# Optimization experiments

Hardware: AMD Instinct MI355X
Metric: run time of the kernel (lower is better)

Reference implementation:

```python
import jax, jax.numpy as jnp
import numpy as np

B, S = 32, 4096
QRYDIM, CTXDIM, ENCDIM = 512, 512, 256


def setup_inputs() -> dict:
    key = jax.random.key(0)
    ks = jax.random.split(key, 8)
    qry = jax.random.normal(ks[0], (B, QRYDIM), dtype=jnp.float32)
    ctx = jax.random.normal(ks[1], (B, S, CTXDIM), dtype=jnp.float32)
    ctx_mask = jax.random.randint(ks[2], (B, S), 0, 2, dtype=jnp.int32)
    # first Linear(qrydim+ctxdim, encdim): split into ctx-part and qry-part
    # (equivalent to concat([ctx, qry]) @ W1^T since concat order is [ctx, qry])
    sc1 = 1.0 / np.sqrt(QRYDIM + CTXDIM)
    Wc = jax.random.uniform(ks[3], (CTXDIM, ENCDIM), jnp.float32, -sc1, sc1)
    Wq = jax.random.uniform(ks[4], (QRYDIM, ENCDIM), jnp.float32, -sc1, sc1)
    b1 = jax.random.uniform(ks[5], (ENCDIM,), jnp.float32, -sc1, sc1)
    sc2 = 1.0 / np.sqrt(ENCDIM)
    w2 = jax.random.uniform(ks[6], (ENCDIM,), jnp.float32, -sc2, sc2)
    b2 = jax.random.uniform(ks[7], (), jnp.float32, -sc2, sc2)
    return {"qry": qry, "ctx": ctx, "ctx_mask": ctx_mask,
            "Wc": Wc, "Wq": Wq, "b1": b1, "w2": w2, "b2": b2}


def reference(qry, ctx, ctx_mask, Wc, Wq, b1, w2, b2):
    # hidden = tanh(concat([ctx, qry_broadcast]) @ W1 + b1), computed without
    # materializing the (B, S, CTXDIM+QRYDIM) concat tensor
    h_ctx = jnp.einsum('bsc,ce->bse', ctx, Wc)          # (B, S, E)
    h_qry = jnp.einsum('bq,qe->be', qry, Wq)            # (B, E)
    h = jnp.tanh(h_ctx + h_qry[:, None, :] + b1)        # (B, S, E)
    scores = jnp.einsum('bse,e->bs', h, w2) + b2        # (B, S)
    # additive log-mask, then softmax over seqlen
    scores = scores + jnp.log(ctx_mask.astype(jnp.float32))
    alphas = jax.nn.softmax(scores, axis=-1)            # (B, S)
    # weighted sum over context (values default to ctx)
    summary = jnp.einsum('bs,bsd->bd', alphas, ctx)     # (B, CTXDIM)
    return alphas, summary, scores
```

## Files before the change

### kernel.cpp

```cpp
#include <hip/hip_runtime.h>
#include <math.h>

#define BB 32
#define SS 4096
#define CD 512
#define ED 256

#define ALPHAS_OFF 0
#define SUMMARY_OFF (BB * SS)
#define SCORES_OFF (BB * SS + BB * CD)

#define NEG_BIG (-1.0e30f)

typedef __attribute__((ext_vector_type(8))) short short8;
typedef __attribute__((ext_vector_type(8))) unsigned short us8;
typedef __attribute__((ext_vector_type(4))) float f32x4;

__device__ __forceinline__ unsigned short f2bf(float f) {
    unsigned u = __float_as_uint(f);
    u += 0x7FFFu + ((u >> 16) & 1u);
    return (unsigned short)(u >> 16);
}
__device__ __forceinline__ float bf2f(unsigned short h) {
    return __uint_as_float(((unsigned)h) << 16);
}
__device__ __forceinline__ float fast_tanh(float x) {
    const float ex = __expf(2.0f * x);
    return 1.0f - __fdividef(2.0f, ex + 1.0f);
}

#define GLOAD_LDS16(g, l) __builtin_amdgcn_global_load_lds( \
    (const __attribute__((address_space(1))) void*)(g),     \
    (__attribute__((address_space(3))) void*)(l), 16, 0, 0)

#define WS_BH_OFF 32768
#define BPLANE 131072

__global__ void k_prep(const float* __restrict__ Wc, unsigned short* __restrict__ Bh,
                       unsigned short* __restrict__ Bl) {
    const int bid = blockIdx.x;
    const int l = threadIdx.x;
    const int e = (bid & 15) * 16 + (l & 15);
    const int kbase = (bid >> 4) * 32 + (l >> 4) * 8;
    const size_t off = ((size_t)bid * 64 + l) * 8;
#pragma unroll
    for (int j = 0; j < 8; ++j) {
        const float f = Wc[(size_t)(kbase + j) * ED + e];
        const unsigned short h = f2bf(f);
        Bh[off + j] = h;
        Bl[off + j] = f2bf(f - bf2f(h));
    }
}

__global__ void k_hq(const float* __restrict__ qry, const float* __restrict__ Wq,
                     const float* __restrict__ b1, float* __restrict__ hq) {
    const int b = blockIdx.x;
    const int e = threadIdx.x;
    __shared__ float qs[CD];
    qs[e] = qry[b * CD + e];
    qs[e + 256] = qry[b * CD + e + 256];
    __syncthreads();
    float acc = b1[e];
#pragma unroll 8
    for (int c = 0; c < CD; ++c) {
        acc = fmaf(qs[c], Wq[c * ED + e], acc);
    }
    hq[b * ED + e] = acc;
}

#define ST 128
__global__ __launch_bounds__(512, 4)
void k_scores(const float* __restrict__ ctx,
              const unsigned short* __restrict__ Bh, const unsigned short* __restrict__ Bl,
              const float* __restrict__ hq, const float* __restrict__ w2,
              const float* __restrict__ b2p, const int* __restrict__ mask,
              float* __restrict__ out) {
    const int b = blockIdx.y;
    const int s0 = blockIdx.x * ST;
    const int tid = threadIdx.x;
    const int w = tid >> 6;
    const int l = tid & 63;
    const int ehalf = w & 1;
    const int mbase = (w >> 1) * 2;

    __shared__ unsigned short AsH[8 * 64 * 8];
    __shared__ unsigned short AsL[8 * 64 * 8];
    __shared__ unsigned short BsH[16 * 64 * 8];
    __shared__ unsigned short BsL[16 * 64 * 8];
    __shared__ float red[2][ST];

    f32x4 acc[2][8];
#pragma unroll
    for (int mi = 0; mi < 2; ++mi)
#pragma unroll
        for (int t = 0; t < 8; ++t) acc[mi][t] = (f32x4)(0.0f);

    const float* ctx_b = ctx + (size_t)(b * SS + s0) * CD;

    const int amt = tid >> 6;
    const int alif = tid & 63;
    const int ar = amt * 16 + (alif & 15);
    const int akg = alif >> 4;
    const float* aptr = ctx_b + (size_t)ar * CD + akg * 8;

    const char* gBplane = (const char*)((w < 4) ? Bh : Bl);
    char* lBplane = (char*)((w < 4) ? BsH : BsL);
    const int bq = (w & 3) * 4096 + l * 16;

    for (int c = 0; c < 16; ++c) {
        __syncthreads();
        {
            const char* gsrc = gBplane + (size_t)c * 16384 + bq;
            char* ldst = lBplane + bq;
            GLOAD_LDS16(gsrc, ldst);
            GLOAD_LDS16(gsrc + 1024, ldst + 1024);
            GLOAD_LDS16(gsrc + 2048, ldst + 2048);
            GLOAD_LDS16(gsrc + 3072, ldst + 3072);
        }
        {
            const float4 v0 = *(const float4*)(aptr + c * 32);
            const float4 v1 = *(const float4*)(aptr + c * 32 + 4);
            const float f[8] = {v0.x, v0.y, v0.z, v0.w, v1.x, v1.y, v1.z, v1.w};
            us8 H, L;
#pragma unroll
            for (int j = 0; j < 8; ++j) {
                const unsigned short h = f2bf(f[j]);
                H[j] = h;
                L[j] = f2bf(f[j] - bf2f(h));
            }
            *(us8*)(&AsH[tid * 8]) = H;
            *(us8*)(&AsL[tid * 8]) = L;
        }
        __syncthreads();

        short8 ah[2], alr[2];
#pragma unroll
        for (int mi = 0; mi < 2; ++mi) {
            const int aoff = ((mbase + mi) * 64 + l) * 8;
            ah[mi] = *(const short8*)(&AsH[aoff]);
            alr[mi] = *(const short8*)(&AsL[aoff]);
        }
#pragma unroll
        for (int et = 0; et < 8; ++et) {
            const int etile = ehalf * 8 + et;
            const int boff = (etile * 64 + l) * 8;
            const short8 bh = *(const short8*)(&BsH[boff]);
            const short8 bl = *(const short8*)(&BsL[boff]);
#pragma unroll
            for (int mi = 0; mi < 2; ++mi) {
                acc[mi][et] = __builtin_amdgcn_mfma_f32_16x16x32_bf16(ah[mi], bh, acc[mi][et], 0, 0, 0);
                acc[mi][et] = __builtin_amdgcn_mfma_f32_16x16x32_bf16(alr[mi], bh, acc[mi][et], 0, 0, 0);
                acc[mi][et] = __builtin_amdgcn_mfma_f32_16x16x32_bf16(ah[mi], bl, acc[mi][et], 0, 0, 0);
            }
        }
    }

    float hqr[8], w2r[8];
#pragma unroll
    for (int t = 0; t < 8; ++t) {
        const int e = (ehalf * 8 + t) * 16 + (l & 15);
        hqr[t] = hq[b * ED + e];
        w2r[t] = w2[e];
    }

#pragma unroll
    for (int mi = 0; mi < 2; ++mi) {
#pragma unroll
        for (int reg = 0; reg < 4; ++reg) {
            float v = 0.0f;
#pragma unroll
            for (int t = 0; t < 8; ++t) {
                v += w2r[t] * fast_tanh(acc[mi][t][reg] + hqr[t]);
            }
            v += __shfl_xor(v, 1, 64);
            v += __shfl_xor(v, 2, 64);
            v += __shfl_xor(v, 4, 64);
            v += __shfl_xor(v, 8, 64);
            if ((l & 15) == 0) {
                const int row = (l >> 4) * 4 + reg;
                red[ehalf][(mbase + mi) * 16 + row] = v;
            }
        }
    }
    __syncthreads();
    if (tid < ST) {
        const int s = s0 + tid;
        float sc = red[0][tid] + red[1][tid] + b2p[0];
        if (mask[b * SS + s] == 0) sc = NEG_BIG;
        out[SCORES_OFF + b * SS + s] = sc;
    }
}

__global__ void k_softmax(float* __restrict__ out) {
    const int b = blockIdx.x;
    const int tid = threadIdx.x;
    const float* sc = out + SCORES_OFF + b * SS;
    float* al = out + ALPHAS_OFF + b * SS;

    __shared__ float red[4];
    __shared__ float bcast;
    const int lane = tid & 63;
    const int wave = tid >> 6;

    float loc[16];
    float mx = -INFINITY;
#pragma unroll
    for (int i = 0; i < 16; ++i) {
        loc[i] = sc[i * 256 + tid];
        mx = fmaxf(mx, loc[i]);
    }
    for (int off = 32; off >= 1; off >>= 1) mx = fmaxf(mx, __shfl_down(mx, off, 64));
    if (lane == 0) red[wave] = mx;
    __syncthreads();
    if (tid == 0) bcast = fmaxf(fmaxf(red[0], red[1]), fmaxf(red[2], red[3]));
    __syncthreads();
    const float mxall = bcast;

    float sum = 0.0f;
#pragma unroll
    for (int i = 0; i < 16; ++i) {
        const float ev = __expf(loc[i] - mxall);
        loc[i] = ev;
        sum += ev;
    }
    for (int off = 32; off >= 1; off >>= 1) sum += __shfl_down(sum, off, 64);
    if (lane == 0) red[wave] = sum;
    __syncthreads();
    if (tid == 0) bcast = red[0] + red[1] + red[2] + red[3];
    __syncthreads();
    const float inv = 1.0f / bcast;

#pragma unroll
    for (int i = 0; i < 16; ++i) al[i * 256 + tid] = loc[i] * inv;
}

__global__ void k_zero(float* __restrict__ out) {
    const int i = blockIdx.x * blockDim.x + threadIdx.x;
    if (i < BB * CD) out[SUMMARY_OFF + i] = 0.0f;
}

#define SROWS 128
__global__ void k_summary(const float* __restrict__ ctx, const float* __restrict__ out_alphas,
                          float* __restrict__ out) {
    const int b = blockIdx.y;
    const int s0 = blockIdx.x * SROWS;
    const int t = threadIdx.x;
    const int sg = t >> 7;
    const int d = (t & 127) * 4;

    __shared__ float al[SROWS];
    if (t < SROWS) al[t] = out_alphas[ALPHAS_OFF + b * SS + s0 + t];
    __syncthreads();

    const float* base = ctx + (size_t)(b * SS + s0 + sg * 64) * CD + d;
    const float* alp = &al[sg * 64];
    float4 a0 = make_float4(0.f, 0.f, 0.f, 0.f);
    float4 a1 = a0, a2 = a0, a3 = a0;
#pragma unroll 2
    for (int i = 0; i < 16; ++i) {
        const int s = i * 4;
        const float w0 = alp[s + 0], w1 = alp[s + 1], w2_ = alp[s + 2], w3 = alp[s + 3];
        if (w0 != 0.0f) {
            const float4 v0 = *(const float4*)(base + (size_t)(s + 0) * CD);
            a0.x = fmaf(w0, v0.x, a0.x); a0.y = fmaf(w0, v0.y, a0.y);
            a0.z = fmaf(w0, v0.z, a0.z); a0.w = fmaf(w0, v0.w, a0.w);
        }
        if (w1 != 0.0f) {
            const float4 v1 = *(const float4*)(base + (size_t)(s + 1) * CD);
            a1.x = fmaf(w1, v1.x, a1.x); a1.y = fmaf(w1, v1.y, a1.y);
            a1.z = fmaf(w1, v1.z, a1.z); a1.w = fmaf(w1, v1.w, a1.w);
        }
        if (w2_ != 0.0f) {
            const float4 v2 = *(const float4*)(base + (size_t)(s + 2) * CD);
            a2.x = fmaf(w2_, v2.x, a2.x); a2.y = fmaf(w2_, v2.y, a2.y);
            a2.z = fmaf(w2_, v2.z, a2.z); a2.w = fmaf(w2_, v2.w, a2.w);
        }
        if (w3 != 0.0f) {
            const float4 v3 = *(const float4*)(base + (size_t)(s + 3) * CD);
            a3.x = fmaf(w3, v3.x, a3.x); a3.y = fmaf(w3, v3.y, a3.y);
            a3.z = fmaf(w3, v3.z, a3.z); a3.w = fmaf(w3, v3.w, a3.w);
        }
    }
    const float rx = (a0.x + a1.x) + (a2.x + a3.x);
    const float ry = (a0.y + a1.y) + (a2.y + a3.y);
    const float rz = (a0.z + a1.z) + (a2.z + a3.z);
    const float rw = (a0.w + a1.w) + (a2.w + a3.w);
    float* dst = out + SUMMARY_OFF + b * CD + d;
    atomicAdd(dst + 0, rx);
    atomicAdd(dst + 1, ry);
    atomicAdd(dst + 2, rz);
    atomicAdd(dst + 3, rw);
}

extern "C" void kernel_launch(void* const* d_in, const int* in_sizes, int n_in,
                              void* d_out, int out_size, void* d_ws, size_t ws_size,
                              hipStream_t stream) {
    const float* qry  = (const float*)d_in[0];
    const float* ctx  = (const float*)d_in[1];
    const int*   msk  = (const int*)d_in[2];
    const float* Wc   = (const float*)d_in[3];
    const float* Wq   = (const float*)d_in[4];
    const float* b1   = (const float*)d_in[5];
    const float* w2   = (const float*)d_in[6];
    const float* b2   = (const float*)d_in[7];
    float* out = (float*)d_out;
    float* hq = (float*)d_ws;
    unsigned short* Bh = (unsigned short*)((char*)d_ws + WS_BH_OFF);
    unsigned short* Bl = Bh + BPLANE;

    k_prep<<<256, 64, 0, stream>>>(Wc, Bh, Bl);
    k_hq<<<BB, ED, 0, stream>>>(qry, Wq, b1, hq);
    k_scores<<<dim3(SS / ST, BB), 512, 0, stream>>>(ctx, Bh, Bl, hq, w2, b2, msk, out);
    k_softmax<<<BB, 256, 0, stream>>>(out);
    k_zero<<<(BB * CD + 255) / 256, 256, 0, stream>>>(out);
    k_summary<<<dim3(SS / SROWS, BB), 256, 0, stream>>>(ctx, out, out);
}
```

Measured before the change: 478.7 us.

## Double-buffer scores GEMM tiles and retile waves to 4x4 MFMA blocks

```diff
diff --git a/kernel.cpp b/kernel.cpp
--- a/kernel.cpp
+++ b/kernel.cpp
@@ -69,7 +69,7 @@
 }
 
 #define ST 128
-__global__ __launch_bounds__(512, 4)
+__global__ __launch_bounds__(512, 2)
 void k_scores(const float* __restrict__ ctx,
               const unsigned short* __restrict__ Bh, const unsigned short* __restrict__ Bl,
               const float* __restrict__ hq, const float* __restrict__ w2,
@@ -80,20 +80,20 @@
     const int tid = threadIdx.x;
     const int w = tid >> 6;
     const int l = tid & 63;
-    const int ehalf = w & 1;
-    const int mbase = (w >> 1) * 2;
-
-    __shared__ unsigned short AsH[8 * 64 * 8];
-    __shared__ unsigned short AsL[8 * 64 * 8];
-    __shared__ unsigned short BsH[16 * 64 * 8];
-    __shared__ unsigned short BsL[16 * 64 * 8];
-    __shared__ float red[2][ST];
-
-    f32x4 acc[2][8];
-#pragma unroll
-    for (int mi = 0; mi < 2; ++mi)
-#pragma unroll
-        for (int t = 0; t < 8; ++t) acc[mi][t] = (f32x4)(0.0f);
+    const int mg = w >> 2;
+    const int eg = w & 3;
+
+    __shared__ unsigned short AsH[2][8 * 64 * 8];
+    __shared__ unsigned short AsL[2][8 * 64 * 8];
+    __shared__ unsigned short BsH[2][16 * 64 * 8];
+    __shared__ unsigned short BsL[2][16 * 64 * 8];
+    __shared__ float red[4][ST];
+
+    f32x4 acc[4][4];
+#pragma unroll
+    for (int mi = 0; mi < 4; ++mi)
+#pragma unroll
+        for (int t = 0; t < 4; ++t) acc[mi][t] = (f32x4)(0.0f);
 
     const float* ctx_b = ctx + (size_t)(b * SS + s0) * CD;
 
@@ -104,23 +104,69 @@
     const float* aptr = ctx_b + (size_t)ar * CD + akg * 8;
 
     const char* gBplane = (const char*)((w < 4) ? Bh : Bl);
-    char* lBplane = (char*)((w < 4) ? BsH : BsL);
+    char* lBbase = (char*)((w < 4) ? &BsH[0][0] : &BsL[0][0]);
     const int bq = (w & 3) * 4096 + l * 16;
 
+    {
+        const float4 v0 = *(const float4*)(aptr);
+        const float4 v1 = *(const float4*)(aptr + 4);
+        const char* gsrc = gBplane + bq;
+        char* ldst = lBbase + bq;
+        GLOAD_LDS16(gsrc, ldst);
+        GLOAD_LDS16(gsrc + 1024, ldst + 1024);
+        GLOAD_LDS16(gsrc + 2048, ldst + 2048);
+        GLOAD_LDS16(gsrc + 3072, ldst + 3072);
+        const float f[8] = {v0.x, v0.y, v0.z, v0.w, v1.x, v1.y, v1.z, v1.w};
+        us8 H, L;
+#pragma unroll
+        for (int j = 0; j < 8; ++j) {
+            const unsigned short h = f2bf(f[j]);
+            H[j] = h;
+            L[j] = f2bf(f[j] - bf2f(h));
+        }
+        *(us8*)(&AsH[0][tid * 8]) = H;
+        *(us8*)(&AsL[0][tid * 8]) = L;
+    }
+    __syncthreads();
+
+    int cur = 0;
     for (int c = 0; c < 16; ++c) {
-        __syncthreads();
-        {
-            const char* gsrc = gBplane + (size_t)c * 16384 + bq;
-            char* ldst = lBplane + bq;
+        const int nxt = cur ^ 1;
+        float4 av0, av1;
+        if (c < 15) {
+            av0 = *(const float4*)(aptr + (c + 1) * 32);
+            av1 = *(const float4*)(aptr + (c + 1) * 32 + 4);
+            const char* gsrc = gBplane + (size_t)(c + 1) * 16384 + bq;
+            char* ldst = lBbase + nxt * 16384 + bq;
             GLOAD_LDS16(gsrc, ldst);
             GLOAD_LDS16(gsrc + 1024, ldst + 1024);
             GLOAD_LDS16(gsrc + 2048, ldst + 2048);
             GLOAD_LDS16(gsrc + 3072, ldst + 3072);
         }
-        {
-            const float4 v0 = *(const float4*)(aptr + c * 32);
-            const float4 v1 = *(const float4*)(aptr + c * 32 + 4);
-            const float f[8] = {v0.x, v0.y, v0.z, v0.w, v1.x, v1.y, v1.z, v1.w};
+
+        short8 ah[4], alr[4];
+#pragma unroll
+        for (int mi = 0; mi < 4; ++mi) {
+            const int aoff = ((mg * 4 + mi) * 64 + l) * 8;
+            ah[mi] = *(const short8*)(&AsH[cur][aoff]);
+            alr[mi] = *(const short8*)(&AsL[cur][aoff]);
+        }
+#pragma unroll
+        for (int t = 0; t < 4; ++t) {
+            const int etile = eg * 4 + t;
+            const int boff = (etile * 64 + l) * 8;
+            const short8 bh = *(const short8*)(&BsH[cur][boff]);
+            const short8 bl = *(const short8*)(&BsL[cur][boff]);
+#pragma unroll
+            for (int mi = 0; mi < 4; ++mi) {
+                acc[mi][t] = __builtin_amdgcn_mfma_f32_16x16x32_bf16(ah[mi], bh, acc[mi][t], 0, 0, 0);
+                acc[mi][t] = __builtin_amdgcn_mfma_f32_16x16x32_bf16(alr[mi], bh, acc[mi][t], 0, 0, 0);
+                acc[mi][t] = __builtin_amdgcn_mfma_f32_16x16x32_bf16(ah[mi], bl, acc[mi][t], 0, 0, 0);
+            }
+        }
+
+        if (c < 15) {
+            const float f[8] = {av0.x, av0.y, av0.z, av0.w, av1.x, av1.y, av1.z, av1.w};
             us8 H, L;
 #pragma unroll
             for (int j = 0; j < 8; ++j) {
@@ -128,48 +174,28 @@
                 H[j] = h;
                 L[j] = f2bf(f[j] - bf2f(h));
             }
-            *(us8*)(&AsH[tid * 8]) = H;
-            *(us8*)(&AsL[tid * 8]) = L;
+            *(us8*)(&AsH[nxt][tid * 8]) = H;
+            *(us8*)(&AsL[nxt][tid * 8]) = L;
         }
         __syncthreads();
-
-        short8 ah[2], alr[2];
-#pragma unroll
-        for (int mi = 0; mi < 2; ++mi) {
-            const int aoff = ((mbase + mi) * 64 + l) * 8;
-            ah[mi] = *(const short8*)(&AsH[aoff]);
-            alr[mi] = *(const short8*)(&AsL[aoff]);
-        }
-#pragma unroll
-        for (int et = 0; et < 8; ++et) {
-            const int etile = ehalf * 8 + et;
-            const int boff = (etile * 64 + l) * 8;
-            const short8 bh = *(const short8*)(&BsH[boff]);
-            const short8 bl = *(const short8*)(&BsL[boff]);
-#pragma unroll
-            for (int mi = 0; mi < 2; ++mi) {
-                acc[mi][et] = __builtin_amdgcn_mfma_f32_16x16x32_bf16(ah[mi], bh, acc[mi][et], 0, 0, 0);
-                acc[mi][et] = __builtin_amdgcn_mfma_f32_16x16x32_bf16(alr[mi], bh, acc[mi][et], 0, 0, 0);
-                acc[mi][et] = __builtin_amdgcn_mfma_f32_16x16x32_bf16(ah[mi], bl, acc[mi][et], 0, 0, 0);
-            }
-        }
-    }
-
-    float hqr[8], w2r[8];
-#pragma unroll
-    for (int t = 0; t < 8; ++t) {
-        const int e = (ehalf * 8 + t) * 16 + (l & 15);
+        cur = nxt;
+    }
+
+    float hqr[4], w2r[4];
+#pragma unroll
+    for (int t = 0; t < 4; ++t) {
+        const int e = (eg * 4 + t) * 16 + (l & 15);
         hqr[t] = hq[b * ED + e];
         w2r[t] = w2[e];
     }
 
 #pragma unroll
-    for (int mi = 0; mi < 2; ++mi) {
+    for (int mi = 0; mi < 4; ++mi) {
 #pragma unroll
         for (int reg = 0; reg < 4; ++reg) {
             float v = 0.0f;
 #pragma unroll
-            for (int t = 0; t < 8; ++t) {
+            for (int t = 0; t < 4; ++t) {
                 v += w2r[t] * fast_tanh(acc[mi][t][reg] + hqr[t]);
             }
             v += __shfl_xor(v, 1, 64);
@@ -178,14 +204,14 @@
             v += __shfl_xor(v, 8, 64);
             if ((l & 15) == 0) {
                 const int row = (l >> 4) * 4 + reg;
-                red[ehalf][(mbase + mi) * 16 + row] = v;
+                red[eg][(mg * 4 + mi) * 16 + row] = v;
             }
         }
     }
     __syncthreads();
     if (tid < ST) {
         const int s = s0 + tid;
-        float sc = red[0][tid] + red[1][tid] + b2p[0];
+        float sc = red[0][tid] + red[1][tid] + red[2][tid] + red[3][tid] + b2p[0];
         if (mask[b * SS + s] == 0) sc = NEG_BIG;
         out[SCORES_OFF + b * SS + s] = sc;
     }
@@ -197,6 +223,12 @@
     const float* sc = out + SCORES_OFF + b * SS;
     float* al = out + ALPHAS_OFF + b * SS;
 
+    {
+        float* sm = out + SUMMARY_OFF + b * CD;
+        sm[tid] = 0.0f;
+        sm[tid + 256] = 0.0f;
+    }
+
     __shared__ float red[4];
     __shared__ float bcast;
     const int lane = tid & 63;
@@ -232,11 +264,6 @@
 
 #pragma unroll
     for (int i = 0; i < 16; ++i) al[i * 256 + tid] = loc[i] * inv;
-}
-
-__global__ void k_zero(float* __restrict__ out) {
-    const int i = blockIdx.x * blockDim.x + threadIdx.x;
-    if (i < BB * CD) out[SUMMARY_OFF + i] = 0.0f;
 }
 
 #define SROWS 128
@@ -312,6 +339,5 @@
     k_hq<<<BB, ED, 0, stream>>>(qry, Wq, b1, hq);
     k_scores<<<dim3(SS / ST, BB), 512, 0, stream>>>(ctx, Bh, Bl, hq, w2, b2, msk, out);
     k_softmax<<<BB, 256, 0, stream>>>(out);
-    k_zero<<<(BB * CD + 255) / 256, 256, 0, stream>>>(out);
     k_summary<<<dim3(SS / SROWS, BB), 256, 0, stream>>>(ctx, out, out);
 }
```

After: 495.6 us. 3.5% more time.
